# Performance work log

Measured on AMD Instinct MI355X. Metric: run time of the kernel, lower is better.

## Reference

```python
import jax, jax.numpy as jnp
import numpy as np

INPUT_SIZE = 128
OUTPUT_SIZE = 128
HIDDEN = 8
BATCH = 1024
N = INPUT_SIZE * OUTPUT_SIZE  # number of tiny subnetworks


def setup_inputs() -> dict:
    key = jax.random.key(0)
    ks = jax.random.split(key, 7)
    s = 0.5  # modest init scale
    return {
        "x": jax.random.normal(ks[0], (BATCH, INPUT_SIZE), dtype=jnp.float32),
        "W1": jax.random.normal(ks[1], (N, HIDDEN, 1), dtype=jnp.float32) * s,
        "b1": jax.random.normal(ks[2], (N, HIDDEN), dtype=jnp.float32) * s,
        "W2": jax.random.normal(ks[3], (N, HIDDEN, HIDDEN), dtype=jnp.float32) * s,
        "b2": jax.random.normal(ks[4], (N, HIDDEN), dtype=jnp.float32) * s,
        "W3": jax.random.normal(ks[5], (N, 1, HIDDEN), dtype=jnp.float32) * s,
        "b3": jax.random.normal(ks[6], (N, 1), dtype=jnp.float32) * s,
    }


def reference(x, W1, b1, W2, b2, W3, b3):
    # x: [B, input_size]. Subnet n = i*output_size + o consumes feature i.
    B = x.shape[0]
    # x.T repeat_interleave(output_size, dim=0).unsqueeze(-1) -> [N, B, 1]
    xe = jnp.repeat(x.T, OUTPUT_SIZE, axis=0)[:, :, None]
    # torch Linear: y = x @ W.T + b, batched over subnet dim n
    h = jax.nn.relu(jnp.einsum('nbi,nhi->nbh', xe, W1) + b1[:, None, :])
    h = jax.nn.relu(jnp.einsum('nbi,nhi->nbh', h, W2) + b2[:, None, :])
    o = jnp.einsum('nbh,noh->nbo', h, W3) + b3[:, None, :]  # [N, B, 1]
    o = o[..., 0].reshape(INPUT_SIZE, OUTPUT_SIZE, B)
    return o.sum(axis=0).T  # [B, output_size]
```

## Files before the change

kernel.cpp:

```cpp
#include <hip/hip_runtime.h>

#define INPUT_SIZE 128
#define OUTPUT_SIZE 128
#define HIDDEN 8
#define BATCH 1024

#define ICH 32
#define IPC (INPUT_SIZE / ICH)
#define TPB 128
#define BPT 8
#define SLOT 60

typedef __fp16 half2v __attribute__((ext_vector_type(2)));

#if defined(__has_builtin)
#if __has_builtin(__builtin_amdgcn_fdot2)
#define HAS_FDOT2 1
#endif
#endif
#ifndef HAS_FDOT2
#define HAS_FDOT2 0
#endif

__global__ void prep_kernel(const float* __restrict__ x,
                            const float* __restrict__ W1,
                            const float* __restrict__ b1,
                            const float* __restrict__ W2,
                            float* __restrict__ xT,
                            unsigned int* __restrict__ W1h,
                            unsigned int* __restrict__ b1h,
                            __fp16* __restrict__ W2h) {
    const int bx = blockIdx.x;
    if (bx < 128) {
        __shared__ float tile[32][33];
        const int i0 = (bx & 3) * 32;
        const int b0 = (bx >> 2) * 32;
        const int tx = threadIdx.x & 31;
        const int ty = threadIdx.x >> 5;
#pragma unroll
        for (int r = ty; r < 32; r += 8)
            tile[r][tx] = x[(b0 + r) * INPUT_SIZE + (i0 + tx)];
        __syncthreads();
#pragma unroll
        for (int r = ty; r < 32; r += 8)
            xT[(i0 + r) * BATCH + (b0 + tx)] = tile[tx][r];
    } else if (bx < 1152) {
        const size_t idx = (size_t)(bx - 128) * 256 + threadIdx.x;
        const float4 v = *(const float4*)(W2 + 4 * idx);
        const half2v a = __builtin_amdgcn_cvt_pkrtz(v.x, v.y);
        const half2v b = __builtin_amdgcn_cvt_pkrtz(v.z, v.w);
        float2 st;
        st.x = __builtin_bit_cast(float, a);
        st.y = __builtin_bit_cast(float, b);
        *(float2*)(W2h + 4 * idx) = st;
    } else if (bx < 1280) {
        const size_t t = (size_t)(bx - 1152) * 256 + threadIdx.x;
        const float4 v = *(const float4*)(W1 + 4 * t);
        W1h[2 * t]     = __builtin_bit_cast(unsigned int, __builtin_amdgcn_cvt_pkrtz(v.x, v.y));
        W1h[2 * t + 1] = __builtin_bit_cast(unsigned int, __builtin_amdgcn_cvt_pkrtz(v.z, v.w));
    } else {
        const size_t t = (size_t)(bx - 1280) * 256 + threadIdx.x;
        const float4 v = *(const float4*)(b1 + 4 * t);
        b1h[2 * t]     = __builtin_bit_cast(unsigned int, __builtin_amdgcn_cvt_pkrtz(v.x, v.y));
        b1h[2 * t + 1] = __builtin_bit_cast(unsigned int, __builtin_amdgcn_cvt_pkrtz(v.z, v.w));
    }
}

__global__ void zero_out_kernel(float* __restrict__ out, int n) {
    int idx = blockIdx.x * blockDim.x + threadIdx.x;
    if (idx < n) out[idx] = 0.0f;
}

template <bool PARTIALS>
__global__ __launch_bounds__(TPB, 4)
void mlpkan_kernel(const float* __restrict__ xT,
                   const unsigned int* __restrict__ W1h,
                   const unsigned int* __restrict__ b1h,
                   const __fp16* __restrict__ W2h, const float* __restrict__ b2,
                   const float* __restrict__ W3, const float* __restrict__ b3,
                   float* __restrict__ partials, float* __restrict__ out) {
    __shared__ float wlds[IPC * SLOT];

    const int o   = blockIdx.x;
    const int ic  = blockIdx.y;
    const int tid = threadIdx.x;

    {
        const int ii  = tid >> 4;
        const int idx = tid & 15;
        if (ii < IPC) {
            const int n = (ic * IPC + ii) * OUTPUT_SIZE + o;
            float* d = &wlds[ii * SLOT];
            if (idx == 0)      *(float4*)(d + 0)  = *(const float4*)((const float*)W1h + (size_t)n * 4);
            else if (idx == 1) *(float4*)(d + 4)  = *(const float4*)((const float*)b1h + (size_t)n * 4);
            else if (idx == 2) *(float4*)(d + 8)  = *(const float4*)(b2 + (size_t)n * 8);
            else if (idx == 3) *(float4*)(d + 12) = *(const float4*)(b2 + (size_t)n * 8 + 4);
            else if (idx == 4) *(float4*)(d + 16) = *(const float4*)(W3 + (size_t)n * 8);
            else if (idx == 5) *(float4*)(d + 20) = *(const float4*)(W3 + (size_t)n * 8 + 4);
            else if (idx == 6) d[24] = b3[n];
            else if (idx >= 8) *(float4*)(d + 28 + 4 * (idx - 8)) =
                *(const float4*)((const char*)W2h + (size_t)n * 128 + (idx - 8) * 16);
        }
    }
    __syncthreads();

    float acc[BPT];
#pragma unroll
    for (int j = 0; j < BPT; ++j) acc[j] = 0.0f;

#pragma unroll 1
    for (int ii = 0; ii < IPC; ++ii) {
        const int i = ic * IPC + ii;
        const float* w = &wlds[ii * SLOT];

        const float4 sA = *(const float4*)(xT + (size_t)i * BATCH + 4 * tid);
        const float4 sB = *(const float4*)(xT + (size_t)i * BATCH + 512 + 4 * tid);
        const float s[BPT] = {sA.x, sA.y, sA.z, sA.w, sB.x, sB.y, sB.z, sB.w};

        const float4 w1q = *(const float4*)(w + 0);
        const float4 b1q = *(const float4*)(w + 4);
        const half2v w1p[4] = {__builtin_bit_cast(half2v, w1q.x), __builtin_bit_cast(half2v, w1q.y),
                               __builtin_bit_cast(half2v, w1q.z), __builtin_bit_cast(half2v, w1q.w)};
        const half2v b1p[4] = {__builtin_bit_cast(half2v, b1q.x), __builtin_bit_cast(half2v, b1q.y),
                               __builtin_bit_cast(half2v, b1q.z), __builtin_bit_cast(half2v, b1q.w)};
        const half2v zero2 = {(__fp16)0.0f, (__fp16)0.0f};

        half2v h1p[BPT][4];
#pragma unroll
        for (int j = 0; j < BPT; ++j) {
            const half2v xx = __builtin_amdgcn_cvt_pkrtz(s[j], s[j]);
#pragma unroll
            for (int q = 0; q < 4; ++q) {
                const half2v v = w1p[q] * xx + b1p[q];
                h1p[j][q] = __builtin_elementwise_max(v, zero2);
            }
        }

        const float4 b2a = *(const float4*)(w + 8);
        const float4 b2b = *(const float4*)(w + 12);
        const float4 w3a = *(const float4*)(w + 16);
        const float4 w3b = *(const float4*)(w + 20);
        const float  b3r = w[24];
        const float b2r[8] = {b2a.x, b2a.y, b2a.z, b2a.w, b2b.x, b2b.y, b2b.z, b2b.w};
        const float w3r[8] = {w3a.x, w3a.y, w3a.z, w3a.w, w3b.x, w3b.y, w3b.z, w3b.w};

        half2v w2p[8][4];
#pragma unroll
        for (int r = 0; r < 8; ++r) {
            const float4 row = *(const float4*)(w + 28 + 4 * r);
            w2p[r][0] = __builtin_bit_cast(half2v, row.x);
            w2p[r][1] = __builtin_bit_cast(half2v, row.y);
            w2p[r][2] = __builtin_bit_cast(half2v, row.z);
            w2p[r][3] = __builtin_bit_cast(half2v, row.w);
        }

#pragma unroll
        for (int j = 0; j < BPT; ++j) {
            float h2[8];
#if HAS_FDOT2
#pragma unroll
            for (int h = 0; h < 8; ++h) {
                float v = b2r[h];
#pragma unroll
                for (int q = 0; q < 4; ++q)
                    v = __builtin_amdgcn_fdot2(w2p[h][q], h1p[j][q], v, false);
                h2[h] = fmaxf(v, 0.0f);
            }
#else
#pragma unroll
            for (int h = 0; h < 8; ++h) {
                float v = b2r[h];
#pragma unroll
                for (int q = 0; q < 4; ++q) {
                    v = fmaf((float)w2p[h][q][0], (float)h1p[j][q][0], v);
                    v = fmaf((float)w2p[h][q][1], (float)h1p[j][q][1], v);
                }
                h2[h] = fmaxf(v, 0.0f);
            }
#endif
            float v3 = b3r;
#pragma unroll
            for (int k = 0; k < 8; ++k)
                v3 = fmaf(w3r[k], h2[k], v3);
            acc[j] += v3;
        }
    }

    if (PARTIALS) {
        float* base = partials + ((size_t)ic * OUTPUT_SIZE + o) * BATCH;
        float4 pa = {acc[0], acc[1], acc[2], acc[3]};
        float4 pb = {acc[4], acc[5], acc[6], acc[7]};
        *(float4*)(base + 4 * tid)       = pa;
        *(float4*)(base + 512 + 4 * tid) = pb;
    } else {
#pragma unroll
        for (int j = 0; j < BPT; ++j) {
            const int b = (j < 4) ? (4 * tid + j) : (512 + 4 * tid + (j - 4));
            atomicAdd(&out[(size_t)b * OUTPUT_SIZE + o], acc[j]);
        }
    }
}

__global__ void reduce_kernel(const float* __restrict__ partials,
                              float* __restrict__ out) {
    __shared__ float tile[32][33];
    const int o0 = blockIdx.x * 32;
    const int b0 = blockIdx.y * 32;
    const int tx = threadIdx.x;
    const int ty = threadIdx.y;
#pragma unroll
    for (int r = ty; r < 32; r += 16) {
        float v = 0.0f;
#pragma unroll
        for (int icc = 0; icc < ICH; ++icc)
            v += partials[((size_t)icc * OUTPUT_SIZE + o0 + r) * BATCH + b0 + tx];
        tile[r][tx] = v;
    }
    __syncthreads();
#pragma unroll
    for (int r = ty; r < 32; r += 16)
        out[(size_t)(b0 + r) * OUTPUT_SIZE + o0 + tx] = tile[tx][r];
}

extern "C" void kernel_launch(void* const* d_in, const int* in_sizes, int n_in,
                              void* d_out, int out_size, void* d_ws, size_t ws_size,
                              hipStream_t stream) {
    const float* x  = (const float*)d_in[0];
    const float* W1 = (const float*)d_in[1];
    const float* b1 = (const float*)d_in[2];
    const float* W2 = (const float*)d_in[3];
    const float* b2 = (const float*)d_in[4];
    const float* W3 = (const float*)d_in[5];
    const float* b3 = (const float*)d_in[6];
    float* out = (float*)d_out;

    const size_t xt_elems   = (size_t)INPUT_SIZE * BATCH;
    const size_t part_elems = (size_t)ICH * OUTPUT_SIZE * BATCH;
    const size_t w2h_bytes  = (size_t)16384 * 64 * sizeof(__fp16);
    const size_t w1h_elems  = (size_t)16384 * 4;
    const size_t need_bytes = (xt_elems + part_elems) * sizeof(float) + w2h_bytes
                            + 2 * w1h_elems * sizeof(unsigned int);

    dim3 mgrid(OUTPUT_SIZE, ICH);

    if (ws_size >= need_bytes) {
        float*        xT       = (float*)d_ws;
        float*        partials = xT + xt_elems;
        __fp16*       W2h      = (__fp16*)(partials + part_elems);
        unsigned int* W1h      = (unsigned int*)((char*)W2h + w2h_bytes);
        unsigned int* b1h      = W1h + w1h_elems;

        prep_kernel<<<1408, 256, 0, stream>>>(x, W1, b1, W2, xT, W1h, b1h, W2h);
        mlpkan_kernel<true><<<mgrid, TPB, 0, stream>>>(xT, W1h, b1h, W2h, b2, W3, b3,
                                                       partials, out);
        dim3 rgrid(OUTPUT_SIZE / 32, BATCH / 32);
        reduce_kernel<<<rgrid, dim3(32, 16), 0, stream>>>(partials, out);
    } else {
        const int nz = BATCH * OUTPUT_SIZE;
        zero_out_kernel<<<(nz + 255) / 256, 256, 0, stream>>>(out, nz);
        if (ws_size >= xt_elems * sizeof(float) + w2h_bytes + 2 * w1h_elems * sizeof(unsigned int)) {
            float*        xT  = (float*)d_ws;
            __fp16*       W2h = (__fp16*)(xT + xt_elems);
            unsigned int* W1h = (unsigned int*)((char*)W2h + w2h_bytes);
            unsigned int* b1h = W1h + w1h_elems;
            prep_kernel<<<1408, 256, 0, stream>>>(x, W1, b1, W2, xT, W1h, b1h, W2h);
            mlpkan_kernel<false><<<mgrid, TPB, 0, stream>>>(xT, W1h, b1h, W2h, b2, W3, b3,
                                                            nullptr, out);
        }
    }
}
```

Baseline: 108.4 us.

## Replace partials buffer and reduce kernel with atomic accumulation and pinned weights

The main path no longer writes per-chunk partial sums to a workspace and runs a separate reduce kernel. Each block now atomically adds its results into the output, which is zeroed first with a memset. The weight values are pinned in registers with empty asm constraints, and the batch loop is split into two halves of four to reduce register pressure. A naive fp32 fallback kernel is added for small workspaces. In exchange the change adds 32-way atomic contention on each output element and nondeterministic summation order.

Measured after the change: 281.9 us. +160.1%, slower.

```diff
diff --git a/kernel.cpp b/kernel.cpp
--- a/kernel.cpp
+++ b/kernel.cpp
@@ -13,6 +13,8 @@
 
 typedef __fp16 half2v __attribute__((ext_vector_type(2)));
 
+#define PINU(x) asm volatile("" : "+v"(x))
+
 #if defined(__has_builtin)
 #if __has_builtin(__builtin_amdgcn_fdot2)
 #define HAS_FDOT2 1
@@ -21,6 +23,10 @@
 #ifndef HAS_FDOT2
 #define HAS_FDOT2 0
 #endif
+
+static __device__ __forceinline__ half2v bch2(unsigned int u) {
+    return __builtin_bit_cast(half2v, u);
+}
 
 __global__ void prep_kernel(const float* __restrict__ x,
                             const float* __restrict__ W1,
@@ -66,19 +72,13 @@
     }
 }
 
-__global__ void zero_out_kernel(float* __restrict__ out, int n) {
-    int idx = blockIdx.x * blockDim.x + threadIdx.x;
-    if (idx < n) out[idx] = 0.0f;
-}
-
-template <bool PARTIALS>
 __global__ __launch_bounds__(TPB, 4)
 void mlpkan_kernel(const float* __restrict__ xT,
                    const unsigned int* __restrict__ W1h,
                    const unsigned int* __restrict__ b1h,
                    const __fp16* __restrict__ W2h, const float* __restrict__ b2,
                    const float* __restrict__ W3, const float* __restrict__ b3,
-                   float* __restrict__ partials, float* __restrict__ out) {
+                   float* __restrict__ out) {
     __shared__ float wlds[IPC * SLOT];
 
     const int o   = blockIdx.x;
@@ -115,111 +115,133 @@
 
         const float4 sA = *(const float4*)(xT + (size_t)i * BATCH + 4 * tid);
         const float4 sB = *(const float4*)(xT + (size_t)i * BATCH + 512 + 4 * tid);
-        const float s[BPT] = {sA.x, sA.y, sA.z, sA.w, sB.x, sB.y, sB.z, sB.w};
-
-        const float4 w1q = *(const float4*)(w + 0);
-        const float4 b1q = *(const float4*)(w + 4);
-        const half2v w1p[4] = {__builtin_bit_cast(half2v, w1q.x), __builtin_bit_cast(half2v, w1q.y),
-                               __builtin_bit_cast(half2v, w1q.z), __builtin_bit_cast(half2v, w1q.w)};
-        const half2v b1p[4] = {__builtin_bit_cast(half2v, b1q.x), __builtin_bit_cast(half2v, b1q.y),
-                               __builtin_bit_cast(half2v, b1q.z), __builtin_bit_cast(half2v, b1q.w)};
+
+        unsigned int w1u[4], b1u[4];
+        {
+            const uint4 a = *(const uint4*)(w + 0);
+            const uint4 b = *(const uint4*)(w + 4);
+            w1u[0] = a.x; w1u[1] = a.y; w1u[2] = a.z; w1u[3] = a.w;
+            b1u[0] = b.x; b1u[1] = b.y; b1u[2] = b.z; b1u[3] = b.w;
+        }
+#pragma unroll
+        for (int q = 0; q < 4; ++q) { PINU(w1u[q]); PINU(b1u[q]); }
+
+        float b2r[8], w3r[8];
+        {
+            const float4 a = *(const float4*)(w + 8);
+            const float4 b = *(const float4*)(w + 12);
+            const float4 c = *(const float4*)(w + 16);
+            const float4 d = *(const float4*)(w + 20);
+            b2r[0] = a.x; b2r[1] = a.y; b2r[2] = a.z; b2r[3] = a.w;
+            b2r[4] = b.x; b2r[5] = b.y; b2r[6] = b.z; b2r[7] = b.w;
+            w3r[0] = c.x; w3r[1] = c.y; w3r[2] = c.z; w3r[3] = c.w;
+            w3r[4] = d.x; w3r[5] = d.y; w3r[6] = d.z; w3r[7] = d.w;
+        }
+#pragma unroll
+        for (int q = 0; q < 8; ++q) { PINU(b2r[q]); PINU(w3r[q]); }
+        float b3r = w[24];
+        PINU(b3r);
+
+        unsigned int w2u[32];
+#pragma unroll
+        for (int r = 0; r < 8; ++r) {
+            const uint4 row = *(const uint4*)(w + 28 + 4 * r);
+            w2u[4 * r + 0] = row.x; w2u[4 * r + 1] = row.y;
+            w2u[4 * r + 2] = row.z; w2u[4 * r + 3] = row.w;
+        }
+#pragma unroll
+        for (int q = 0; q < 32; ++q) PINU(w2u[q]);
+
         const half2v zero2 = {(__fp16)0.0f, (__fp16)0.0f};
 
-        half2v h1p[BPT][4];
-#pragma unroll
-        for (int j = 0; j < BPT; ++j) {
-            const half2v xx = __builtin_amdgcn_cvt_pkrtz(s[j], s[j]);
-#pragma unroll
-            for (int q = 0; q < 4; ++q) {
-                const half2v v = w1p[q] * xx + b1p[q];
-                h1p[j][q] = __builtin_elementwise_max(v, zero2);
+#pragma unroll
+        for (int jh = 0; jh < 2; ++jh) {
+            const float4 sv = jh ? sB : sA;
+            const float sjs[4] = {sv.x, sv.y, sv.z, sv.w};
+
+            half2v h1p[4][4];
+#pragma unroll
+            for (int j = 0; j < 4; ++j) {
+                const half2v xx = __builtin_amdgcn_cvt_pkrtz(sjs[j], sjs[j]);
+#pragma unroll
+                for (int q = 0; q < 4; ++q) {
+                    const half2v v = bch2(w1u[q]) * xx + bch2(b1u[q]);
+                    h1p[j][q] = __builtin_elementwise_max(v, zero2);
+                }
             }
-        }
-
-        const float4 b2a = *(const float4*)(w + 8);
-        const float4 b2b = *(const float4*)(w + 12);
-        const float4 w3a = *(const float4*)(w + 16);
-        const float4 w3b = *(const float4*)(w + 20);
-        const float  b3r = w[24];
-        const float b2r[8] = {b2a.x, b2a.y, b2a.z, b2a.w, b2b.x, b2b.y, b2b.z, b2b.w};
-        const float w3r[8] = {w3a.x, w3a.y, w3a.z, w3a.w, w3b.x, w3b.y, w3b.z, w3b.w};
-
-        half2v w2p[8][4];
-#pragma unroll
-        for (int r = 0; r < 8; ++r) {
-            const float4 row = *(const float4*)(w + 28 + 4 * r);
-            w2p[r][0] = __builtin_bit_cast(half2v, row.x);
-            w2p[r][1] = __builtin_bit_cast(half2v, row.y);
-            w2p[r][2] = __builtin_bit_cast(half2v, row.z);
-            w2p[r][3] = __builtin_bit_cast(half2v, row.w);
-        }
-
-#pragma unroll
-        for (int j = 0; j < BPT; ++j) {
-            float h2[8];
+
+#pragma unroll
+            for (int j = 0; j < 4; ++j) {
+                float h2[8];
 #if HAS_FDOT2
 #pragma unroll
-            for (int h = 0; h < 8; ++h) {
-                float v = b2r[h];
-#pragma unroll
-                for (int q = 0; q < 4; ++q)
-                    v = __builtin_amdgcn_fdot2(w2p[h][q], h1p[j][q], v, false);
-                h2[h] = fmaxf(v, 0.0f);
+                for (int h = 0; h < 8; ++h) {
+                    float v = b2r[h];
+#pragma unroll
+                    for (int q = 0; q < 4; ++q)
+                        v = __builtin_amdgcn_fdot2(bch2(w2u[4 * h + q]), h1p[j][q], v, false);
+                    h2[h] = fmaxf(v, 0.0f);
+                }
+#else
+#pragma unroll
+                for (int h = 0; h < 8; ++h) {
+                    float v = b2r[h];
+#pragma unroll
+                    for (int q = 0; q < 4; ++q) {
+                        const half2v wv = bch2(w2u[4 * h + q]);
+                        v = fmaf((float)wv[0], (float)h1p[j][q][0], v);
+                        v = fmaf((float)wv[1], (float)h1p[j][q][1], v);
+                    }
+                    h2[h] = fmaxf(v, 0.0f);
+                }
+#endif
+                float v3 = b3r;
+#pragma unroll
+                for (int k = 0; k < 8; ++k)
+                    v3 = fmaf(w3r[k], h2[k], v3);
+                acc[jh * 4 + j] += v3;
             }
-#else
-#pragma unroll
-            for (int h = 0; h < 8; ++h) {
-                float v = b2r[h];
-#pragma unroll
-                for (int q = 0; q < 4; ++q) {
-                    v = fmaf((float)w2p[h][q][0], (float)h1p[j][q][0], v);
-                    v = fmaf((float)w2p[h][q][1], (float)h1p[j][q][1], v);
-                }
-                h2[h] = fmaxf(v, 0.0f);
-            }
-#endif
-            float v3 = b3r;
+        }
+    }
+
+#pragma unroll
+    for (int j = 0; j < BPT; ++j) {
+        const int b = (j < 4) ? (4 * tid + j) : (512 + 4 * tid + (j - 4));
+        atomicAdd(&out[(size_t)b * OUTPUT_SIZE + o], acc[j]);
+    }
+}
+
+__global__ __launch_bounds__(256, 2)
+void mlpkan_naive(const float* __restrict__ x,
+                  const float* __restrict__ W1, const float* __restrict__ b1,
+                  const float* __restrict__ W2, const float* __restrict__ b2,
+                  const float* __restrict__ W3, const float* __restrict__ b3,
+                  float* __restrict__ out) {
+    const int o = blockIdx.x;
+    const int b = blockIdx.y * 256 + threadIdx.x;
+    float acc = 0.0f;
+    for (int i = 0; i < INPUT_SIZE; ++i) {
+        const int n = i * OUTPUT_SIZE + o;
+        const float s = x[b * INPUT_SIZE + i];
+        float h1[8], h2[8];
+#pragma unroll
+        for (int k = 0; k < 8; ++k)
+            h1[k] = fmaxf(fmaf(W1[(size_t)n * 8 + k], s, b1[(size_t)n * 8 + k]), 0.0f);
+#pragma unroll
+        for (int h = 0; h < 8; ++h) {
+            float v = b2[(size_t)n * 8 + h];
 #pragma unroll
             for (int k = 0; k < 8; ++k)
-                v3 = fmaf(w3r[k], h2[k], v3);
-            acc[j] += v3;
-        }
-    }
-
-    if (PARTIALS) {
-        float* base = partials + ((size_t)ic * OUTPUT_SIZE + o) * BATCH;
-        float4 pa = {acc[0], acc[1], acc[2], acc[3]};
-        float4 pb = {acc[4], acc[5], acc[6], acc[7]};
-        *(float4*)(base + 4 * tid)       = pa;
-        *(float4*)(base + 512 + 4 * tid) = pb;
-    } else {
-#pragma unroll
-        for (int j = 0; j < BPT; ++j) {
-            const int b = (j < 4) ? (4 * tid + j) : (512 + 4 * tid + (j - 4));
-            atomicAdd(&out[(size_t)b * OUTPUT_SIZE + o], acc[j]);
-        }
-    }
-}
-
-__global__ void reduce_kernel(const float* __restrict__ partials,
-                              float* __restrict__ out) {
-    __shared__ float tile[32][33];
-    const int o0 = blockIdx.x * 32;
-    const int b0 = blockIdx.y * 32;
-    const int tx = threadIdx.x;
-    const int ty = threadIdx.y;
-#pragma unroll
-    for (int r = ty; r < 32; r += 16) {
-        float v = 0.0f;
-#pragma unroll
-        for (int icc = 0; icc < ICH; ++icc)
-            v += partials[((size_t)icc * OUTPUT_SIZE + o0 + r) * BATCH + b0 + tx];
-        tile[r][tx] = v;
-    }
-    __syncthreads();
-#pragma unroll
-    for (int r = ty; r < 32; r += 16)
-        out[(size_t)(b0 + r) * OUTPUT_SIZE + o0 + tx] = tile[tx][r];
+                v = fmaf(W2[(size_t)n * 64 + h * 8 + k], h1[k], v);
+            h2[h] = fmaxf(v, 0.0f);
+        }
+        float v = b3[n];
+#pragma unroll
+        for (int k = 0; k < 8; ++k)
+            v = fmaf(W3[(size_t)n * 8 + k], h2[k], v);
+        acc += v;
+    }
+    out[(size_t)b * OUTPUT_SIZE + o] = acc;
 }
 
 extern "C" void kernel_launch(void* const* d_in, const int* in_sizes, int n_in,
@@ -234,38 +256,24 @@
     const float* b3 = (const float*)d_in[6];
     float* out = (float*)d_out;
 
-    const size_t xt_elems   = (size_t)INPUT_SIZE * BATCH;
-    const size_t part_elems = (size_t)ICH * OUTPUT_SIZE * BATCH;
-    const size_t w2h_bytes  = (size_t)16384 * 64 * sizeof(__fp16);
-    const size_t w1h_elems  = (size_t)16384 * 4;
-    const size_t need_bytes = (xt_elems + part_elems) * sizeof(float) + w2h_bytes
+    const size_t xt_elems  = (size_t)INPUT_SIZE * BATCH;
+    const size_t w2h_bytes = (size_t)16384 * 64 * sizeof(__fp16);
+    const size_t w1h_elems = (size_t)16384 * 4;
+    const size_t need_bytes = xt_elems * sizeof(float) + w2h_bytes
                             + 2 * w1h_elems * sizeof(unsigned int);
 
-    dim3 mgrid(OUTPUT_SIZE, ICH);
-
     if (ws_size >= need_bytes) {
-        float*        xT       = (float*)d_ws;
-        float*        partials = xT + xt_elems;
-        __fp16*       W2h      = (__fp16*)(partials + part_elems);
-        unsigned int* W1h      = (unsigned int*)((char*)W2h + w2h_bytes);
-        unsigned int* b1h      = W1h + w1h_elems;
-
+        float*        xT  = (float*)d_ws;
+        __fp16*       W2h = (__fp16*)(xT + xt_elems);
+        unsigned int* W1h = (unsigned int*)((char*)W2h + w2h_bytes);
+        unsigned int* b1h = W1h + w1h_elems;
+
+        hipMemsetAsync(d_out, 0, (size_t)BATCH * OUTPUT_SIZE * sizeof(float), stream);
         prep_kernel<<<1408, 256, 0, stream>>>(x, W1, b1, W2, xT, W1h, b1h, W2h);
-        mlpkan_kernel<true><<<mgrid, TPB, 0, stream>>>(xT, W1h, b1h, W2h, b2, W3, b3,
-                                                       partials, out);
-        dim3 rgrid(OUTPUT_SIZE / 32, BATCH / 32);
-        reduce_kernel<<<rgrid, dim3(32, 16), 0, stream>>>(partials, out);
+        mlpkan_kernel<<<dim3(OUTPUT_SIZE, ICH), TPB, 0, stream>>>(
+            xT, W1h, b1h, W2h, b2, W3, b3, out);
     } else {
-        const int nz = BATCH * OUTPUT_SIZE;
-        zero_out_kernel<<<(nz + 255) / 256, 256, 0, stream>>>(out, nz);
-        if (ws_size >= xt_elems * sizeof(float) + w2h_bytes + 2 * w1h_elems * sizeof(unsigned int)) {
-            float*        xT  = (float*)d_ws;
-            __fp16*       W2h = (__fp16*)(xT + xt_elems);
-            unsigned int* W1h = (unsigned int*)((char*)W2h + w2h_bytes);
-            unsigned int* b1h = W1h + w1h_elems;
-            prep_kernel<<<1408, 256, 0, stream>>>(x, W1, b1, W2, xT, W1h, b1h, W2h);
-            mlpkan_kernel<false><<<mgrid, TPB, 0, stream>>>(xT, W1h, b1h, W2h, b2, W3, b3,
-                                                            nullptr, out);
-        }
-    }
-}
+        mlpkan_naive<<<dim3(OUTPUT_SIZE, BATCH / 256), 256, 0, stream>>>(
+            x, W1, b1, W2, b2, W3, b3, out);
+    }
+}
```
